# Optimization experiments

Measured on AMD Instinct MI355X. Metric: run time of the kernel, lower is better.

The kernel has to match this reference:

```python
import jax, jax.numpy as jnp
import numpy as np

B, H, W = 512, 15, 15
DF, DP, DV, DD = 64, 32, 64, 32
PM = 16
NUM_LINE = 442503  # get_total_num_line_encoding(11)


def fake_quant(x, scale=128., num_bits=8, floor=False):
    qmin = float(-(2 ** (num_bits - 1)))
    qmax = float(2 ** (num_bits - 1) - 1)
    xs = jnp.clip(x * scale, qmin, qmax)
    q = jnp.floor(xs) if floor else jnp.round(xs)
    q = xs + jax.lax.stop_gradient(q - xs)  # straight-through estimator
    return q / scale


def qw(w):  # LinearBlock quant=True weight: int8 at scale 128
    return fake_quant(w, 128., 8)


def qb(b):  # LinearBlock quant=True bias: int32 at scale 128*128
    return fake_quant(b, 128. * 128., 32)


def setup_inputs() -> dict:
    key = jax.random.key(0)
    ks = jax.random.split(key, 24)
    n = lambda k, shape, s=0.1: jax.random.normal(k, shape, dtype=jnp.float32) * s
    return {
        'line_encoding': jax.random.randint(ks[0], (B, 4, H, W), 0, NUM_LINE, dtype=jnp.int32),
        'emb': n(ks[1], (NUM_LINE, DF), 0.5),
        'dw_w': n(ks[2], (DD, 3, 3)),
        'dw_b': n(ks[3], (DD,)),
        'pw1_w': n(ks[4], (DP * 2, DF)), 'pw1_b': n(ks[5], (DP * 2,)),
        'pw2_w': n(ks[6], (PM * DP + PM, DP * 2)), 'pw2_b': n(ks[7], (PM * DP + PM,)),
        'pout_w': n(ks[8], (PM,), 0.2), 'pout_b': n(ks[9], (1,), 0.2),
        'star_up1_w': n(ks[10], (4, DV, DF)), 'star_up1_b': n(ks[11], (4, DV)),
        'star_up2_w': n(ks[12], (4, DV, DF)), 'star_up2_b': n(ks[13], (4, DV)),
        'star_down_w': n(ks[14], (4, DV, DV)), 'star_down_b': n(ks[15], (4, DV)),
        'vl1_w': n(ks[16], (DV, DF + 4 * DV)), 'vl1_b': n(ks[17], (DV,)),
        'vl2_w': n(ks[18], (DV, DV)), 'vl2_b': n(ks[19], (DV,)),
        'vl3_w': n(ks[20], (3, DV)), 'vl3_b': n(ks[21], (3,)),
    }


def _star(x, w1, b1, w2, b2, w3, b3):
    # x: [B,R,DF]; weights [R,DV,DF] (per-region parameter gather)
    x1 = jnp.einsum('brc,rdc->brd', x, qw(w1)) + qb(b1)[None]
    x2 = jnp.einsum('brc,rdc->brd', x, qw(w2)) + qb(b2)[None]
    h = jax.nn.relu(x1) * x2  # star operation
    return jnp.einsum('brc,rdc->brd', h, qw(w3)) + qb(b3)[None]


def _forward(line_encoding, emb, dw_w, dw_b, pw1_w, pw1_b, pw2_w, pw2_b,
             pout_w, pout_b, star_up1_w, star_up1_b, star_up2_w, star_up2_b,
             star_down_w, star_down_b, vl1_w, vl1_b, vl2_w, vl2_b, vl3_w, vl3_b):
    # ---- feature: embedding gather + quant + direction mean ----
    f = emb[line_encoding]                       # [B,4,H,W,DF]
    f = jnp.clip(f, -16., 16.)
    f = fake_quant(f, 32., 16)
    f = jax.nn.relu(jnp.mean(f, axis=1))         # [B,H,W,DF]
    f = jnp.transpose(f, (0, 3, 1, 2))           # [B,DF,H,W]
    # ---- depthwise 3x3 conv, quant='pixel-dwconv-floor' ----
    x = fake_quant(f[:, :DD] * 4., 128., 16)
    wq = fake_quant(dw_w, 65536., 16)
    bq = fake_quant(dw_b, 128., 16)
    xp = jnp.pad(x, ((0, 0), (0, 0), (1, 1), (1, 1)))
    pat = jnp.stack([xp[:, :, dy:dy + H, dx:dx + W]
                     for dy in range(3) for dx in range(3)], axis=2)  # [B,DD,9,H,W]
    prod = fake_quant(pat * wq.reshape(1, DD, 9, 1, 1), 128., 32, floor=True)
    conv = jax.nn.relu(prod.sum(axis=2) + bq.reshape(1, DD, 1, 1))
    feat_dw = fake_quant(conv, 128., 16)
    feat_dir = fake_quant(f[:, DD:], 128., 16)
    feature = jnp.concatenate([feat_dw, feat_dir], axis=1)  # [B,DF,H,W]
    # ---- global and 3x3 regional sums ----
    feature_sum = fake_quant(feature.sum(axis=(2, 3)) / 256., 128., 32, floor=True)
    Hs = [0, H // 3 + (H % 3 == 2), H // 3 * 2 + (H % 3 > 0), H]
    Ws = [0, W // 3 + (W % 3 == 2), W // 3 * 2 + (W % 3 > 0), W]
    regions = jnp.stack([feature[:, :, Hs[i]:Hs[i + 1], Ws[j]:Ws[j + 1]].sum(axis=(2, 3))
                         for i in range(3) for j in range(3)], axis=1)  # [B,9,DF]
    regions = fake_quant(regions / 32., 128., 32, floor=True)
    # ---- policy: dynamic per-sample pointwise conv ----
    h = jax.nn.relu(feature_sum @ qw(pw1_w).T + qb(pw1_b))
    o = h @ qw(pw2_w).T + qb(pw2_b)                         # [B, PM*DP+PM]
    pw = fake_quant(o[:, :PM * DP], 128. * 128., 16, floor=True).reshape(-1, PM, DP)
    pin = fake_quant(feature[:, :DP], 128., 16)             # [B,DP,H,W]
    pol = jnp.einsum('bchw,bic->bihw', pin, pw)             # grouped conv, groups=B
    pbias = o[:, PM * DP:].reshape(-1, PM, 1, 1)
    pol = jax.nn.relu(pol + pbias)
    policy = jnp.einsum('bihw,i->bhw', pol, pout_w)[:, None] + pout_b[0]  # [B,1,H,W]
    # ---- value: corner/edge/center star blocks over 9 regions ----
    idx = jnp.array([0, 1, 0, 1, 2, 1, 0, 1, 0])  # 0=corner,1=edge,2=center
    v = _star(regions, star_up1_w[idx], star_up1_b[idx], star_up2_w[idx],
              star_up2_b[idx], star_down_w[idx], star_down_b[idx])  # [B,9,DV]
    fq8 = lambda t: fake_quant(t, 128., 8, floor=True)
    def avg4(a, b, c, d):
        a, b, c, d = fq8(a), fq8(b), fq8(c), fq8(d)
        ab = fq8((a + b + 1. / 128.) / 2.)
        cd = fq8((c + d + 1. / 128.) / 2.)
        return fq8((ab + cd + 1. / 128.) / 2.)
    quads = jnp.stack([avg4(v[:, 0], v[:, 1], v[:, 3], v[:, 4]),
                       avg4(v[:, 1], v[:, 2], v[:, 4], v[:, 5]),
                       avg4(v[:, 3], v[:, 4], v[:, 6], v[:, 7]),
                       avg4(v[:, 4], v[:, 5], v[:, 7], v[:, 8])], axis=1)  # [B,4,DV]
    qidx = jnp.array([3, 3, 3, 3])  # value_quad shared across quadrants
    vq = _star(quads, star_up1_w[qidx], star_up1_b[qidx], star_up2_w[qidx],
               star_up2_b[qidx], star_down_w[qidx], star_down_b[qidx])  # [B,4,DV]
    value = jnp.concatenate([feature_sum, vq.reshape(vq.shape[0], -1)], axis=1)  # [B,320]
    value = jax.nn.relu(value @ qw(vl1_w).T + qb(vl1_b))
    value = jax.nn.relu(value @ qw(vl2_w).T + qb(vl2_b))
    value = value @ qw(vl3_w).T + qb(vl3_b)                 # [B,3]
    return value, policy


def reference(line_encoding, emb, dw_w, dw_b, pw1_w, pw1_b, pw2_w, pw2_b,
              pout_w, pout_b, star_up1_w, star_up1_b, star_up2_w, star_up2_b,
              star_down_w, star_down_b, vl1_w, vl1_b, vl2_w, vl2_b, vl3_w, vl3_b):
    return _forward(line_encoding, emb, dw_w, dw_b, pw1_w, pw1_b, pw2_w, pw2_b,
                    pout_w, pout_b, star_up1_w, star_up1_b, star_up2_w, star_up2_b,
                    star_down_w, star_down_b, vl1_w, vl1_b, vl2_w, vl2_b, vl3_w, vl3_b)
```

## Files before the change

kernel.cpp:

```cpp
#include <hip/hip_runtime.h>

#define NPOS 225
#define FSTR 227

__device__ __forceinline__ float qw8(float w) {
  return rintf(fminf(fmaxf(w * 128.f, -128.f), 127.f)) * 0.0078125f;
}
__device__ __forceinline__ float qb32(float b) {
  return rintf(b * 16384.f) * 6.103515625e-05f;
}
__device__ __forceinline__ float fq8f(float v) {
  return floorf(fminf(fmaxf(v * 128.f, -128.f), 127.f)) * 0.0078125f;
}
__device__ __forceinline__ float qdir(float v) {
  return rintf(fminf(fmaxf(v, -16.f), 16.f) * 32.f) * 0.03125f;
}

__global__ __launch_bounds__(256, 2)
void nnue_fused(const int* __restrict__ line,
                const float* __restrict__ emb,
                const float* __restrict__ dw_w,  const float* __restrict__ dw_b,
                const float* __restrict__ pw1_w, const float* __restrict__ pw1_b,
                const float* __restrict__ pw2_w, const float* __restrict__ pw2_b,
                const float* __restrict__ pout_w,const float* __restrict__ pout_b,
                const float* __restrict__ su1w,  const float* __restrict__ su1b,
                const float* __restrict__ su2w,  const float* __restrict__ su2b,
                const float* __restrict__ sdw,   const float* __restrict__ sdb,
                const float* __restrict__ vl1w,  const float* __restrict__ vl1b,
                const float* __restrict__ vl2w,  const float* __restrict__ vl2b,
                const float* __restrict__ vl3w,  const float* __restrict__ vl3b,
                float* __restrict__ out)
{
  __shared__ float fbuf[64 * FSTR];
  __shared__ float sreg[9 * 64];
  __shared__ float sfsum[64];
  __shared__ float shh[64];
  __shared__ float sobuf[528];
  __shared__ float spwq[512];
  __shared__ float hstar[9 * 64];
  __shared__ float vstar[9 * 64];
  __shared__ float squads[4 * 64];
  __shared__ float shq[4 * 64];
  __shared__ float svq[4 * 64];
  __shared__ float sv1[64];
  __shared__ float sv2[64];

  const int tid  = threadIdx.x;
  const int b    = blockIdx.x;
  const int wid  = tid >> 6;
  const int lane = tid & 63;
  const int* le  = line + b * 4 * NPOS;

  for (int p = wid; p < NPOS; p += 8) {
    const int p2 = p + 4;
    const bool h2 = (p2 < NPOS);
    int i0 = le[p], i1 = le[NPOS + p], i2 = le[2 * NPOS + p], i3 = le[3 * NPOS + p];
    int j0 = i0, j1 = i1, j2 = i2, j3 = i3;
    if (h2) { j0 = le[p2]; j1 = le[NPOS + p2]; j2 = le[2 * NPOS + p2]; j3 = le[3 * NPOS + p2]; }
    float a0 = emb[i0 * 64 + lane], a1 = emb[i1 * 64 + lane];
    float a2 = emb[i2 * 64 + lane], a3 = emb[i3 * 64 + lane];
    float c0 = emb[j0 * 64 + lane], c1 = emb[j1 * 64 + lane];
    float c2 = emb[j2 * 64 + lane], c3 = emb[j3 * 64 + lane];
    fbuf[lane * FSTR + p] = fmaxf((qdir(a0) + qdir(a1) + qdir(a2) + qdir(a3)) * 0.25f, 0.f);
    if (h2)
      fbuf[lane * FSTR + p2] = fmaxf((qdir(c0) + qdir(c1) + qdir(c2) + qdir(c3)) * 0.25f, 0.f);
  }
  __syncthreads();

  {
    const int cc = tid >> 3;
    const int pg = tid & 7;
    float wq9[9];
#pragma unroll
    for (int t = 0; t < 9; ++t)
      wq9[t] = rintf(fminf(fmaxf(dw_w[cc * 9 + t] * 65536.f, -32768.f), 32767.f)) * 1.52587890625e-05f;
    const float bq = rintf(fminf(fmaxf(dw_b[cc] * 128.f, -32768.f), 32767.f)) * 0.0078125f;
    float outr[29];
#pragma unroll
    for (int k = 0; k < 29; ++k) {
      const int p = pg + 8 * k;
      if (p < NPOS) {
        const int y0 = p / 15, x0 = p - y0 * 15;
        float s = 0.f;
#pragma unroll
        for (int dy = 0; dy < 3; ++dy)
#pragma unroll
          for (int dx = 0; dx < 3; ++dx) {
            const int y = y0 + dy - 1, x = x0 + dx - 1;
            float xv = 0.f;
            if ((unsigned)y < 15u && (unsigned)x < 15u) xv = 4.f * fbuf[cc * FSTR + y * 15 + x];
            s += floorf(xv * wq9[dy * 3 + dx] * 128.f) * 0.0078125f;
          }
        s = fmaxf(s + bq, 0.f);
        outr[k] = fminf(s, 255.9921875f);
      } else outr[k] = 0.f;
    }
    __syncthreads();
#pragma unroll
    for (int k = 0; k < 29; ++k) {
      const int p = pg + 8 * k;
      if (p < NPOS) fbuf[cc * FSTR + p] = outr[k];
    }
  }
  __syncthreads();

  if (tid < 64) {
    float tot = 0.f;
#pragma unroll
    for (int rh = 0; rh < 3; ++rh)
#pragma unroll
      for (int rw = 0; rw < 3; ++rw) {
        float rs = 0.f;
        for (int y = rh * 5; y < rh * 5 + 5; ++y)
          for (int x = rw * 5; x < rw * 5 + 5; ++x)
            rs += fbuf[tid * FSTR + y * 15 + x];
        sreg[(rh * 3 + rw) * 64 + tid] = floorf(rs * 4.f) * 0.0078125f;
        tot += rs;
      }
    sfsum[tid] = floorf(tot * 0.5f) * 0.0078125f;
  }
  __syncthreads();

  if (tid < 64) {
    const float4* wr = (const float4*)(pw1_w + tid * 64);
    float acc = 0.f;
#pragma unroll
    for (int c4 = 0; c4 < 16; ++c4) {
      float4 w = wr[c4];
      acc += sfsum[c4 * 4 + 0] * qw8(w.x);
      acc += sfsum[c4 * 4 + 1] * qw8(w.y);
      acc += sfsum[c4 * 4 + 2] * qw8(w.z);
      acc += sfsum[c4 * 4 + 3] * qw8(w.w);
    }
    acc += qb32(pw1_b[tid]);
    shh[tid] = fmaxf(acc, 0.f);
  }
  __syncthreads();
  for (int j = tid; j < 528; j += 256) {
    const float4* wr = (const float4*)(pw2_w + j * 64);
    float acc = 0.f;
#pragma unroll
    for (int c4 = 0; c4 < 16; ++c4) {
      float4 w = wr[c4];
      acc += shh[c4 * 4 + 0] * qw8(w.x);
      acc += shh[c4 * 4 + 1] * qw8(w.y);
      acc += shh[c4 * 4 + 2] * qw8(w.z);
      acc += shh[c4 * 4 + 3] * qw8(w.w);
    }
    acc += qb32(pw2_b[j]);
    sobuf[j] = acc;
    if (j < 512)
      spwq[j] = floorf(fminf(fmaxf(acc * 16384.f, -32768.f), 32767.f)) * 6.103515625e-05f;
  }
  __syncthreads();

  if (tid < NPOS) {
    float pinv[32];
#pragma unroll
    for (int c = 0; c < 32; ++c) pinv[c] = fbuf[c * FSTR + tid];
    float acc = 0.f;
#pragma unroll
    for (int i = 0; i < 16; ++i) {
      float s = 0.f;
#pragma unroll
      for (int c = 0; c < 32; ++c) s += pinv[c] * spwq[i * 32 + c];
      s = fmaxf(s + sobuf[512 + i], 0.f);
      acc += s * pout_w[i];
    }
    out[1536 + b * NPOS + tid] = acc + pout_b[0];
  }

  {
    const int g = tid >> 6;
    const int d = tid & 63;
    int ty, rA, rB, rC, rD;
    if (g == 0)      { ty = 0; rA = 0; rB = 2; rC = 6; rD = 8; }
    else if (g == 1) { ty = 1; rA = 1; rB = 3; rC = 5; rD = 7; }
    else             { ty = 2; rA = 4; rB = 4; rC = 4; rD = 4; }
    const float4* w1r = (const float4*)(su1w + ty * 4096 + d * 64);
    const float4* w2r = (const float4*)(su2w + ty * 4096 + d * 64);
    float aA1 = 0, aB1 = 0, aC1 = 0, aD1 = 0, aA2 = 0, aB2 = 0, aC2 = 0, aD2 = 0;
#pragma unroll 4
    for (int c4 = 0; c4 < 16; ++c4) {
      float4 w1 = w1r[c4], w2 = w2r[c4];
      float q1[4] = {qw8(w1.x), qw8(w1.y), qw8(w1.z), qw8(w1.w)};
      float q2[4] = {qw8(w2.x), qw8(w2.y), qw8(w2.z), qw8(w2.w)};
#pragma unroll
      for (int u = 0; u < 4; ++u) {
        const int c = c4 * 4 + u;
        float xA = sreg[rA * 64 + c], xB = sreg[rB * 64 + c];
        float xC = sreg[rC * 64 + c], xD = sreg[rD * 64 + c];
        aA1 += xA * q1[u]; aB1 += xB * q1[u]; aC1 += xC * q1[u]; aD1 += xD * q1[u];
        aA2 += xA * q2[u]; aB2 += xB * q2[u]; aC2 += xC * q2[u]; aD2 += xD * q2[u];
      }
    }
    const float bb1 = qb32(su1b[ty * 64 + d]);
    const float bb2 = qb32(su2b[ty * 64 + d]);
    hstar[rA * 64 + d] = fmaxf(aA1 + bb1, 0.f) * (aA2 + bb2);
    hstar[rB * 64 + d] = fmaxf(aB1 + bb1, 0.f) * (aB2 + bb2);
    hstar[rC * 64 + d] = fmaxf(aC1 + bb1, 0.f) * (aC2 + bb2);
    hstar[rD * 64 + d] = fmaxf(aD1 + bb1, 0.f) * (aD2 + bb2);
    __syncthreads();
    const float4* wdr = (const float4*)(sdw + ty * 4096 + d * 64);
    float dA = 0, dB = 0, dC = 0, dD = 0;
#pragma unroll 4
    for (int c4 = 0; c4 < 16; ++c4) {
      float4 w = wdr[c4];
      float q[4] = {qw8(w.x), qw8(w.y), qw8(w.z), qw8(w.w)};
#pragma unroll
      for (int u = 0; u < 4; ++u) {
        const int c = c4 * 4 + u;
        dA += hstar[rA * 64 + c] * q[u]; dB += hstar[rB * 64 + c] * q[u];
        dC += hstar[rC * 64 + c] * q[u]; dD += hstar[rD * 64 + c] * q[u];
      }
    }
    const float bd = qb32(sdb[ty * 64 + d]);
    vstar[rA * 64 + d] = dA + bd;
    vstar[rB * 64 + d] = dB + bd;
    vstar[rC * 64 + d] = dC + bd;
    vstar[rD * 64 + d] = dD + bd;
  }
  __syncthreads();

  {
    const int g = tid >> 6, d = tid & 63;
    int r0, r1, r2v, r3v;
    if (g == 0)      { r0 = 0; r1 = 1; r2v = 3; r3v = 4; }
    else if (g == 1) { r0 = 1; r1 = 2; r2v = 4; r3v = 5; }
    else if (g == 2) { r0 = 3; r1 = 4; r2v = 6; r3v = 7; }
    else             { r0 = 4; r1 = 5; r2v = 7; r3v = 8; }
    float a  = fq8f(vstar[r0 * 64 + d]);
    float bb = fq8f(vstar[r1 * 64 + d]);
    float cc = fq8f(vstar[r2v * 64 + d]);
    float dd = fq8f(vstar[r3v * 64 + d]);
    float ab = fq8f((a + bb + 0.0078125f) * 0.5f);
    float cd = fq8f((cc + dd + 0.0078125f) * 0.5f);
    squads[g * 64 + d] = fq8f((ab + cd + 0.0078125f) * 0.5f);
  }
  __syncthreads();

  {
    const int g = tid >> 6, d = tid & 63;
    const float4* w1r = (const float4*)(su1w + 3 * 4096 + d * 64);
    const float4* w2r = (const float4*)(su2w + 3 * 4096 + d * 64);
    float a1 = 0.f, a2 = 0.f;
#pragma unroll 4
    for (int c4 = 0; c4 < 16; ++c4) {
      float4 w1 = w1r[c4], w2 = w2r[c4];
      float q1[4] = {qw8(w1.x), qw8(w1.y), qw8(w1.z), qw8(w1.w)};
      float q2[4] = {qw8(w2.x), qw8(w2.y), qw8(w2.z), qw8(w2.w)};
#pragma unroll
      for (int u = 0; u < 4; ++u) {
        float xq = squads[g * 64 + c4 * 4 + u];
        a1 += xq * q1[u];
        a2 += xq * q2[u];
      }
    }
    shq[g * 64 + d] = fmaxf(a1 + qb32(su1b[192 + d]), 0.f) * (a2 + qb32(su2b[192 + d]));
    __syncthreads();
    const float4* wdr = (const float4*)(sdw + 3 * 4096 + d * 64);
    float ad = 0.f;
#pragma unroll 4
    for (int c4 = 0; c4 < 16; ++c4) {
      float4 w = wdr[c4];
      float q[4] = {qw8(w.x), qw8(w.y), qw8(w.z), qw8(w.w)};
#pragma unroll
      for (int u = 0; u < 4; ++u) ad += shq[g * 64 + c4 * 4 + u] * q[u];
    }
    svq[g * 64 + d] = ad + qb32(sdb[192 + d]);
  }
  __syncthreads();

  if (tid < 64) {
    const float4* wr = (const float4*)(vl1w + tid * 320);
    float acc = 0.f;
#pragma unroll 4
    for (int k4 = 0; k4 < 16; ++k4) {
      float4 w = wr[k4];
      acc += sfsum[k4 * 4 + 0] * qw8(w.x);
      acc += sfsum[k4 * 4 + 1] * qw8(w.y);
      acc += sfsum[k4 * 4 + 2] * qw8(w.z);
      acc += sfsum[k4 * 4 + 3] * qw8(w.w);
    }
#pragma unroll 4
    for (int k4 = 16; k4 < 80; ++k4) {
      float4 w = wr[k4];
      const int base = k4 * 4 - 64;
      acc += svq[base + 0] * qw8(w.x);
      acc += svq[base + 1] * qw8(w.y);
      acc += svq[base + 2] * qw8(w.z);
      acc += svq[base + 3] * qw8(w.w);
    }
    acc += qb32(vl1b[tid]);
    sv1[tid] = fmaxf(acc, 0.f);
  }
  __syncthreads();
  if (tid < 64) {
    const float4* wr = (const float4*)(vl2w + tid * 64);
    float acc = 0.f;
#pragma unroll 4
    for (int k4 = 0; k4 < 16; ++k4) {
      float4 w = wr[k4];
      acc += sv1[k4 * 4 + 0] * qw8(w.x);
      acc += sv1[k4 * 4 + 1] * qw8(w.y);
      acc += sv1[k4 * 4 + 2] * qw8(w.z);
      acc += sv1[k4 * 4 + 3] * qw8(w.w);
    }
    acc += qb32(vl2b[tid]);
    sv2[tid] = fmaxf(acc, 0.f);
  }
  __syncthreads();
  if (tid < 3) {
    const float* wr = vl3w + tid * 64;
    float acc = 0.f;
#pragma unroll
    for (int k = 0; k < 64; ++k) acc += sv2[k] * qw8(wr[k]);
    out[b * 3 + tid] = acc + qb32(vl3b[tid]);
  }
}

extern "C" void kernel_launch(void* const* d_in, const int* in_sizes, int n_in,
                              void* d_out, int out_size, void* d_ws, size_t ws_size,
                              hipStream_t stream) {
  (void)in_sizes; (void)n_in; (void)out_size; (void)d_ws; (void)ws_size;
  nnue_fused<<<512, 256, 0, stream>>>(
      (const int*)d_in[0],  (const float*)d_in[1],
      (const float*)d_in[2],  (const float*)d_in[3],
      (const float*)d_in[4],  (const float*)d_in[5],
      (const float*)d_in[6],  (const float*)d_in[7],
      (const float*)d_in[8],  (const float*)d_in[9],
      (const float*)d_in[10], (const float*)d_in[11],
      (const float*)d_in[12], (const float*)d_in[13],
      (const float*)d_in[14], (const float*)d_in[15],
      (const float*)d_in[16], (const float*)d_in[17],
      (const float*)d_in[18], (const float*)d_in[19],
      (const float*)d_in[20], (const float*)d_in[21],
      (float*)d_out);
}
```

Before: 285.2 us.

## Pre-quantize weights in a prep kernel and switch feature map to integer ushort

Adds a prep kernel that quantizes all weights and biases into a workspace once per call, so the main kernel no longer repeats the quantization math in every block. The feature map moves from float to unsigned short fixed-point, and the depthwise conv becomes integer arithmetic. This halves shared memory use and allows 3 blocks per CU. The embedding gather is batched using indices staged in LDS with readfirstlane, and the region sums are spread across all threads. The cost is an extra kernel launch, and the exactness of the integer rewrite depends on the fixed-point equivalences holding.

```diff
diff --git a/kernel.cpp b/kernel.cpp
--- a/kernel.cpp
+++ b/kernel.cpp
@@ -1,7 +1,27 @@
 #include <hip/hip_runtime.h>
 
 #define NPOS 225
-#define FSTR 227
+#define FSTR 226
+
+#define OFF_PW1Q 0
+#define OFF_PW2Q 4096
+#define OFF_SU1Q 37888
+#define OFF_SU2Q 54272
+#define OFF_SDQ  70656
+#define OFF_VL1Q 87040
+#define OFF_VL2Q 107520
+#define OFF_VL3Q 111616
+#define OFF_PW1B 111808
+#define OFF_PW2B 111872
+#define OFF_SU1B 112400
+#define OFF_SU2B 112656
+#define OFF_SDB  112912
+#define OFF_VL1B 113168
+#define OFF_VL2B 113232
+#define OFF_VL3B 113296
+#define OFF_DWW  113300
+#define OFF_DWB  113588
+#define WS_TOTAL 113620
 
 __device__ __forceinline__ float qw8(float w) {
   return rintf(fminf(fmaxf(w * 128.f, -128.f), 127.f)) * 0.0078125f;
@@ -12,36 +32,70 @@
 __device__ __forceinline__ float fq8f(float v) {
   return floorf(fminf(fmaxf(v * 128.f, -128.f), 127.f)) * 0.0078125f;
 }
-__device__ __forceinline__ float qdir(float v) {
-  return rintf(fminf(fmaxf(v, -16.f), 16.f) * 32.f) * 0.03125f;
-}
-
-__global__ __launch_bounds__(256, 2)
-void nnue_fused(const int* __restrict__ line,
-                const float* __restrict__ emb,
-                const float* __restrict__ dw_w,  const float* __restrict__ dw_b,
-                const float* __restrict__ pw1_w, const float* __restrict__ pw1_b,
-                const float* __restrict__ pw2_w, const float* __restrict__ pw2_b,
-                const float* __restrict__ pout_w,const float* __restrict__ pout_b,
-                const float* __restrict__ su1w,  const float* __restrict__ su1b,
-                const float* __restrict__ su2w,  const float* __restrict__ su2b,
-                const float* __restrict__ sdw,   const float* __restrict__ sdb,
-                const float* __restrict__ vl1w,  const float* __restrict__ vl1b,
-                const float* __restrict__ vl2w,  const float* __restrict__ vl2b,
-                const float* __restrict__ vl3w,  const float* __restrict__ vl3b,
-                float* __restrict__ out)
+__device__ __forceinline__ float qd32(float v) {
+  return rintf(fminf(fmaxf(v, -16.f), 16.f) * 32.f);
+}
+
+__global__ void nnue_prep(const float* __restrict__ pw1_w, const float* __restrict__ pw1_b,
+                          const float* __restrict__ pw2_w, const float* __restrict__ pw2_b,
+                          const float* __restrict__ su1w,  const float* __restrict__ su1b,
+                          const float* __restrict__ su2w,  const float* __restrict__ su2b,
+                          const float* __restrict__ sdw,   const float* __restrict__ sdb,
+                          const float* __restrict__ vl1w,  const float* __restrict__ vl1b,
+                          const float* __restrict__ vl2w,  const float* __restrict__ vl2b,
+                          const float* __restrict__ vl3w,  const float* __restrict__ vl3b,
+                          const float* __restrict__ dw_w,  const float* __restrict__ dw_b,
+                          float* __restrict__ wsf, int* __restrict__ wsi)
 {
-  __shared__ float fbuf[64 * FSTR];
-  __shared__ float sreg[9 * 64];
+  const int i = blockIdx.x * 256 + threadIdx.x;
+  if (i < 111808) {
+    const float* src; int off;
+    if      (i < 4096)   { src = pw1_w; off = 0; }
+    else if (i < 37888)  { src = pw2_w; off = 4096; }
+    else if (i < 54272)  { src = su1w;  off = 37888; }
+    else if (i < 70656)  { src = su2w;  off = 54272; }
+    else if (i < 87040)  { src = sdw;   off = 70656; }
+    else if (i < 107520) { src = vl1w;  off = 87040; }
+    else if (i < 111616) { src = vl2w;  off = 107520; }
+    else                 { src = vl3w;  off = 111616; }
+    wsf[i] = qw8(src[i - off]);
+  } else if (i < 113299) {
+    const int j = i - 111808;
+    const float* src; int off;
+    if      (j < 64)   { src = pw1_b; off = 0; }
+    else if (j < 592)  { src = pw2_b; off = 64; }
+    else if (j < 848)  { src = su1b;  off = 592; }
+    else if (j < 1104) { src = su2b;  off = 848; }
+    else if (j < 1360) { src = sdb;   off = 1104; }
+    else if (j < 1424) { src = vl1b;  off = 1360; }
+    else if (j < 1488) { src = vl2b;  off = 1424; }
+    else               { src = vl3b;  off = 1488; }
+    wsf[i] = qb32(src[j - off]);
+  } else if (i >= 113300 && i < 113588) {
+    wsi[i] = (int)rintf(fminf(fmaxf(dw_w[i - 113300] * 65536.f, -32768.f), 32767.f));
+  } else if (i >= 113588 && i < 113620) {
+    wsi[i] = (int)rintf(fminf(fmaxf(dw_b[i - 113588] * 128.f, -32768.f), 32767.f));
+  }
+}
+
+__global__ __launch_bounds__(256, 3)
+void nnue_main(const int* __restrict__ line, const float* __restrict__ emb,
+               const float* __restrict__ pout_w, const float* __restrict__ pout_b,
+               const float* __restrict__ wsf, const int* __restrict__ wsi,
+               float* __restrict__ out)
+{
+  __shared__ unsigned short fbuf[64 * FSTR];
+  __shared__ int sle[900];
+  __shared__ float sreg[576];
   __shared__ float sfsum[64];
   __shared__ float shh[64];
   __shared__ float sobuf[528];
   __shared__ float spwq[512];
-  __shared__ float hstar[9 * 64];
-  __shared__ float vstar[9 * 64];
-  __shared__ float squads[4 * 64];
-  __shared__ float shq[4 * 64];
-  __shared__ float svq[4 * 64];
+  __shared__ float hstar[576];
+  __shared__ float vstar[576];
+  __shared__ float squads[256];
+  __shared__ float shq[256];
+  __shared__ float svq[256];
   __shared__ float sv1[64];
   __shared__ float sv2[64];
 
@@ -51,103 +105,132 @@
   const int lane = tid & 63;
   const int* le  = line + b * 4 * NPOS;
 
-  for (int p = wid; p < NPOS; p += 8) {
-    const int p2 = p + 4;
-    const bool h2 = (p2 < NPOS);
-    int i0 = le[p], i1 = le[NPOS + p], i2 = le[2 * NPOS + p], i3 = le[3 * NPOS + p];
-    int j0 = i0, j1 = i1, j2 = i2, j3 = i3;
-    if (h2) { j0 = le[p2]; j1 = le[NPOS + p2]; j2 = le[2 * NPOS + p2]; j3 = le[3 * NPOS + p2]; }
-    float a0 = emb[i0 * 64 + lane], a1 = emb[i1 * 64 + lane];
-    float a2 = emb[i2 * 64 + lane], a3 = emb[i3 * 64 + lane];
-    float c0 = emb[j0 * 64 + lane], c1 = emb[j1 * 64 + lane];
-    float c2 = emb[j2 * 64 + lane], c3 = emb[j3 * 64 + lane];
-    fbuf[lane * FSTR + p] = fmaxf((qdir(a0) + qdir(a1) + qdir(a2) + qdir(a3)) * 0.25f, 0.f);
-    if (h2)
-      fbuf[lane * FSTR + p2] = fmaxf((qdir(c0) + qdir(c1) + qdir(c2) + qdir(c3)) * 0.25f, 0.f);
+  for (int i = tid; i < 900; i += 256) sle[i] = le[i];
+  __syncthreads();
+
+  const int start = (wid * NPOS) >> 2;
+  const int end   = ((wid + 1) * NPOS) >> 2;
+  for (int p0 = start; p0 < end; p0 += 8) {
+    float vv[32];
+#pragma unroll
+    for (int j = 0; j < 8; ++j) {
+      int pp = p0 + j; if (pp >= end) pp = end - 1;
+#pragma unroll
+      for (int d = 0; d < 4; ++d) {
+        const int idx = __builtin_amdgcn_readfirstlane(sle[d * NPOS + pp]);
+        vv[j * 4 + d] = emb[(size_t)(unsigned)idx * 64u + (unsigned)lane];
+      }
+    }
+#pragma unroll
+    for (int j = 0; j < 8; ++j) {
+      const int pp = p0 + j;
+      if (pp < end) {
+        float s = qd32(vv[4 * j]) + qd32(vv[4 * j + 1]) + qd32(vv[4 * j + 2]) + qd32(vv[4 * j + 3]);
+        fbuf[lane * FSTR + pp] = (unsigned short)fmaxf(s, 0.f);
+      }
+    }
   }
   __syncthreads();
 
   {
     const int cc = tid >> 3;
     const int pg = tid & 7;
-    float wq9[9];
-#pragma unroll
-    for (int t = 0; t < 9; ++t)
-      wq9[t] = rintf(fminf(fmaxf(dw_w[cc * 9 + t] * 65536.f, -32768.f), 32767.f)) * 1.52587890625e-05f;
-    const float bq = rintf(fminf(fmaxf(dw_b[cc] * 128.f, -32768.f), 32767.f)) * 0.0078125f;
-    float outr[29];
+    int w9[9];
+#pragma unroll
+    for (int t = 0; t < 9; ++t) w9[t] = wsi[OFF_DWW + cc * 9 + t];
+    const int bqi = wsi[OFF_DWB + cc];
+    const unsigned short* frow = &fbuf[cc * FSTR];
+    int outr[29];
 #pragma unroll
     for (int k = 0; k < 29; ++k) {
       const int p = pg + 8 * k;
+      int res = 0;
       if (p < NPOS) {
-        const int y0 = p / 15, x0 = p - y0 * 15;
-        float s = 0.f;
-#pragma unroll
-        for (int dy = 0; dy < 3; ++dy)
+        const int y0 = (p * 2185) >> 15;
+        const int x0 = p - y0 * 15;
+        const int ym = (y0 > 0), yp = (y0 < 14), xm = (x0 > 0), xp = (x0 < 14);
+        int acc = 0;
+#pragma unroll
+        for (int dy = 0; dy < 3; ++dy) {
+          const int vy = (dy == 0) ? ym : ((dy == 2) ? yp : 1);
 #pragma unroll
           for (int dx = 0; dx < 3; ++dx) {
-            const int y = y0 + dy - 1, x = x0 + dx - 1;
-            float xv = 0.f;
-            if ((unsigned)y < 15u && (unsigned)x < 15u) xv = 4.f * fbuf[cc * FSTR + y * 15 + x];
-            s += floorf(xv * wq9[dy * 3 + dx] * 128.f) * 0.0078125f;
+            const int vx = (dx == 0) ? xm : ((dx == 2) ? xp : 1);
+            int q = p + (dy - 1) * 15 + (dx - 1);
+            q = (q < 0) ? 0 : ((q > 224) ? 224 : q);
+            int kk = frow[q];
+            kk = (vy && vx) ? kk : 0;
+            acc += (kk * 4 * w9[dy * 3 + dx]) >> 16;
           }
-        s = fmaxf(s + bq, 0.f);
-        outr[k] = fminf(s, 255.9921875f);
-      } else outr[k] = 0.f;
+        }
+        res = acc + bqi;
+        res = res < 0 ? 0 : res;
+        res = res > 32767 ? 32767 : res;
+      }
+      outr[k] = res;
     }
     __syncthreads();
 #pragma unroll
     for (int k = 0; k < 29; ++k) {
       const int p = pg + 8 * k;
-      if (p < NPOS) fbuf[cc * FSTR + p] = outr[k];
-    }
-  }
-  __syncthreads();
-
+      if (p < NPOS) fbuf[cc * FSTR + p] = (unsigned short)outr[k];
+    }
+  }
+  __syncthreads();
+
+  {
+    int* sregKi = (int*)sreg;
+    for (int task = tid; task < 576; task += 256) {
+      const int r = task >> 6, c = task & 63;
+      const int rh = (r * 11) >> 5;
+      const int rw = r - rh * 3;
+      const unsigned short* fr = &fbuf[c * FSTR + rh * 75 + rw * 5];
+      int K = 0;
+#pragma unroll
+      for (int y = 0; y < 5; ++y)
+#pragma unroll
+        for (int x = 0; x < 5; ++x) K += fr[y * 15 + x];
+      sregKi[task] = K;
+    }
+  }
+  __syncthreads();
   if (tid < 64) {
-    float tot = 0.f;
-#pragma unroll
-    for (int rh = 0; rh < 3; ++rh)
-#pragma unroll
-      for (int rw = 0; rw < 3; ++rw) {
-        float rs = 0.f;
-        for (int y = rh * 5; y < rh * 5 + 5; ++y)
-          for (int x = rw * 5; x < rw * 5 + 5; ++x)
-            rs += fbuf[tid * FSTR + y * 15 + x];
-        sreg[(rh * 3 + rw) * 64 + tid] = floorf(rs * 4.f) * 0.0078125f;
-        tot += rs;
-      }
-    sfsum[tid] = floorf(tot * 0.5f) * 0.0078125f;
+    int* sregKi = (int*)sreg;
+    int Ks[9], tot = 0;
+#pragma unroll
+    for (int r = 0; r < 9; ++r) { Ks[r] = sregKi[r * 64 + tid]; tot += Ks[r]; }
+#pragma unroll
+    for (int r = 0; r < 9; ++r) sreg[r * 64 + tid] = (float)(Ks[r] >> 5) * 0.0078125f;
+    sfsum[tid] = (float)(tot >> 8) * 0.0078125f;
   }
   __syncthreads();
 
   if (tid < 64) {
-    const float4* wr = (const float4*)(pw1_w + tid * 64);
+    const float4* wr = (const float4*)(wsf + OFF_PW1Q + tid * 64);
     float acc = 0.f;
 #pragma unroll
     for (int c4 = 0; c4 < 16; ++c4) {
       float4 w = wr[c4];
-      acc += sfsum[c4 * 4 + 0] * qw8(w.x);
-      acc += sfsum[c4 * 4 + 1] * qw8(w.y);
-      acc += sfsum[c4 * 4 + 2] * qw8(w.z);
-      acc += sfsum[c4 * 4 + 3] * qw8(w.w);
-    }
-    acc += qb32(pw1_b[tid]);
-    shh[tid] = fmaxf(acc, 0.f);
+      acc += sfsum[c4 * 4 + 0] * w.x;
+      acc += sfsum[c4 * 4 + 1] * w.y;
+      acc += sfsum[c4 * 4 + 2] * w.z;
+      acc += sfsum[c4 * 4 + 3] * w.w;
+    }
+    shh[tid] = fmaxf(acc + wsf[OFF_PW1B + tid], 0.f);
   }
   __syncthreads();
   for (int j = tid; j < 528; j += 256) {
-    const float4* wr = (const float4*)(pw2_w + j * 64);
+    const float4* wr = (const float4*)(wsf + OFF_PW2Q + j * 64);
     float acc = 0.f;
 #pragma unroll
     for (int c4 = 0; c4 < 16; ++c4) {
       float4 w = wr[c4];
-      acc += shh[c4 * 4 + 0] * qw8(w.x);
-      acc += shh[c4 * 4 + 1] * qw8(w.y);
-      acc += shh[c4 * 4 + 2] * qw8(w.z);
-      acc += shh[c4 * 4 + 3] * qw8(w.w);
-    }
-    acc += qb32(pw2_b[j]);
+      acc += shh[c4 * 4 + 0] * w.x;
+      acc += shh[c4 * 4 + 1] * w.y;
+      acc += shh[c4 * 4 + 2] * w.z;
+      acc += shh[c4 * 4 + 3] * w.w;
+    }
+    acc += wsf[OFF_PW2B + j];
     sobuf[j] = acc;
     if (j < 512)
       spwq[j] = floorf(fminf(fmaxf(acc * 16384.f, -32768.f), 32767.f)) * 6.103515625e-05f;
@@ -157,7 +240,7 @@
   if (tid < NPOS) {
     float pinv[32];
 #pragma unroll
-    for (int c = 0; c < 32; ++c) pinv[c] = fbuf[c * FSTR + tid];
+    for (int c = 0; c < 32; ++c) pinv[c] = (float)fbuf[c * FSTR + tid] * 0.0078125f;
     float acc = 0.f;
 #pragma unroll
     for (int i = 0; i < 16; ++i) {
@@ -177,14 +260,14 @@
     if (g == 0)      { ty = 0; rA = 0; rB = 2; rC = 6; rD = 8; }
     else if (g == 1) { ty = 1; rA = 1; rB = 3; rC = 5; rD = 7; }
     else             { ty = 2; rA = 4; rB = 4; rC = 4; rD = 4; }
-    const float4* w1r = (const float4*)(su1w + ty * 4096 + d * 64);
-    const float4* w2r = (const float4*)(su2w + ty * 4096 + d * 64);
+    const float4* w1r = (const float4*)(wsf + OFF_SU1Q + ty * 4096 + d * 64);
+    const float4* w2r = (const float4*)(wsf + OFF_SU2Q + ty * 4096 + d * 64);
     float aA1 = 0, aB1 = 0, aC1 = 0, aD1 = 0, aA2 = 0, aB2 = 0, aC2 = 0, aD2 = 0;
 #pragma unroll 4
     for (int c4 = 0; c4 < 16; ++c4) {
       float4 w1 = w1r[c4], w2 = w2r[c4];
-      float q1[4] = {qw8(w1.x), qw8(w1.y), qw8(w1.z), qw8(w1.w)};
-      float q2[4] = {qw8(w2.x), qw8(w2.y), qw8(w2.z), qw8(w2.w)};
+      float q1[4] = {w1.x, w1.y, w1.z, w1.w};
+      float q2[4] = {w2.x, w2.y, w2.z, w2.w};
 #pragma unroll
       for (int u = 0; u < 4; ++u) {
         const int c = c4 * 4 + u;
@@ -194,19 +277,19 @@
         aA2 += xA * q2[u]; aB2 += xB * q2[u]; aC2 += xC * q2[u]; aD2 += xD * q2[u];
       }
     }
-    const float bb1 = qb32(su1b[ty * 64 + d]);
-    const float bb2 = qb32(su2b[ty * 64 + d]);
+    const float bb1 = wsf[OFF_SU1B + ty * 64 + d];
+    const float bb2 = wsf[OFF_SU2B + ty * 64 + d];
     hstar[rA * 64 + d] = fmaxf(aA1 + bb1, 0.f) * (aA2 + bb2);
     hstar[rB * 64 + d] = fmaxf(aB1 + bb1, 0.f) * (aB2 + bb2);
     hstar[rC * 64 + d] = fmaxf(aC1 + bb1, 0.f) * (aC2 + bb2);
     hstar[rD * 64 + d] = fmaxf(aD1 + bb1, 0.f) * (aD2 + bb2);
     __syncthreads();
-    const float4* wdr = (const float4*)(sdw + ty * 4096 + d * 64);
+    const float4* wdr = (const float4*)(wsf + OFF_SDQ + ty * 4096 + d * 64);
     float dA = 0, dB = 0, dC = 0, dD = 0;
 #pragma unroll 4
     for (int c4 = 0; c4 < 16; ++c4) {
       float4 w = wdr[c4];
-      float q[4] = {qw8(w.x), qw8(w.y), qw8(w.z), qw8(w.w)};
+      float q[4] = {w.x, w.y, w.z, w.w};
 #pragma unroll
       for (int u = 0; u < 4; ++u) {
         const int c = c4 * 4 + u;
@@ -214,7 +297,7 @@
         dC += hstar[rC * 64 + c] * q[u]; dD += hstar[rD * 64 + c] * q[u];
       }
     }
-    const float bd = qb32(sdb[ty * 64 + d]);
+    const float bd = wsf[OFF_SDB + ty * 64 + d];
     vstar[rA * 64 + d] = dA + bd;
     vstar[rB * 64 + d] = dB + bd;
     vstar[rC * 64 + d] = dC + bd;
@@ -241,99 +324,96 @@
 
   {
     const int g = tid >> 6, d = tid & 63;
-    const float4* w1r = (const float4*)(su1w + 3 * 4096 + d * 64);
-    const float4* w2r = (const float4*)(su2w + 3 * 4096 + d * 64);
+    const float4* w1r = (const float4*)(wsf + OFF_SU1Q + 3 * 4096 + d * 64);
+    const float4* w2r = (const float4*)(wsf + OFF_SU2Q + 3 * 4096 + d * 64);
     float a1 = 0.f, a2 = 0.f;
 #pragma unroll 4
     for (int c4 = 0; c4 < 16; ++c4) {
       float4 w1 = w1r[c4], w2 = w2r[c4];
-      float q1[4] = {qw8(w1.x), qw8(w1.y), qw8(w1.z), qw8(w1.w)};
-      float q2[4] = {qw8(w2.x), qw8(w2.y), qw8(w2.z), qw8(w2.w)};
-#pragma unroll
-      for (int u = 0; u < 4; ++u) {
-        float xq = squads[g * 64 + c4 * 4 + u];
-        a1 += xq * q1[u];
-        a2 += xq * q2[u];
-      }
-    }
-    shq[g * 64 + d] = fmaxf(a1 + qb32(su1b[192 + d]), 0.f) * (a2 + qb32(su2b[192 + d]));
+      float xq0 = squads[g * 64 + c4 * 4 + 0], xq1 = squads[g * 64 + c4 * 4 + 1];
+      float xq2 = squads[g * 64 + c4 * 4 + 2], xq3 = squads[g * 64 + c4 * 4 + 3];
+      a1 += xq0 * w1.x + xq1 * w1.y + xq2 * w1.z + xq3 * w1.w;
+      a2 += xq0 * w2.x + xq1 * w2.y + xq2 * w2.z + xq3 * w2.w;
+    }
+    shq[g * 64 + d] = fmaxf(a1 + wsf[OFF_SU1B + 192 + d], 0.f) * (a2 + wsf[OFF_SU2B + 192 + d]);
     __syncthreads();
-    const float4* wdr = (const float4*)(sdw + 3 * 4096 + d * 64);
+    const float4* wdr = (const float4*)(wsf + OFF_SDQ + 3 * 4096 + d * 64);
     float ad = 0.f;
 #pragma unroll 4
     for (int c4 = 0; c4 < 16; ++c4) {
       float4 w = wdr[c4];
-      float q[4] = {qw8(w.x), qw8(w.y), qw8(w.z), qw8(w.w)};
-#pragma unroll
-      for (int u = 0; u < 4; ++u) ad += shq[g * 64 + c4 * 4 + u] * q[u];
-    }
-    svq[g * 64 + d] = ad + qb32(sdb[192 + d]);
+      ad += shq[g * 64 + c4 * 4 + 0] * w.x + shq[g * 64 + c4 * 4 + 1] * w.y
+          + shq[g * 64 + c4 * 4 + 2] * w.z + shq[g * 64 + c4 * 4 + 3] * w.w;
+    }
+    svq[g * 64 + d] = ad + wsf[OFF_SDB + 192 + d];
   }
   __syncthreads();
 
   if (tid < 64) {
-    const float4* wr = (const float4*)(vl1w + tid * 320);
+    const float4* wr = (const float4*)(wsf + OFF_VL1Q + tid * 320);
     float acc = 0.f;
 #pragma unroll 4
     for (int k4 = 0; k4 < 16; ++k4) {
       float4 w = wr[k4];
-      acc += sfsum[k4 * 4 + 0] * qw8(w.x);
-      acc += sfsum[k4 * 4 + 1] * qw8(w.y);
-      acc += sfsum[k4 * 4 + 2] * qw8(w.z);
-      acc += sfsum[k4 * 4 + 3] * qw8(w.w);
+      acc += sfsum[k4 * 4 + 0] * w.x;
+      acc += sfsum[k4 * 4 + 1] * w.y;
+      acc += sfsum[k4 * 4 + 2] * w.z;
+      acc += sfsum[k4 * 4 + 3] * w.w;
     }
 #pragma unroll 4
     for (int k4 = 16; k4 < 80; ++k4) {
       float4 w = wr[k4];
       const int base = k4 * 4 - 64;
-      acc += svq[base + 0] * qw8(w.x);
-      acc += svq[base + 1] * qw8(w.y);
-      acc += svq[base + 2] * qw8(w.z);
-      acc += svq[base + 3] * qw8(w.w);
-    }
-    acc += qb32(vl1b[tid]);
-    sv1[tid] = fmaxf(acc, 0.f);
+      acc += svq[base + 0] * w.x;
+      acc += svq[base + 1] * w.y;
+      acc += svq[base + 2] * w.z;
+      acc += svq[base + 3] * w.w;
+    }
+    sv1[tid] = fmaxf(acc + wsf[OFF_VL1B + tid], 0.f);
   }
   __syncthreads();
   if (tid < 64) {
-    const float4* wr = (const float4*)(vl2w + tid * 64);
+    const float4* wr = (const float4*)(wsf + OFF_VL2Q + tid * 64);
     float acc = 0.f;
 #pragma unroll 4
     for (int k4 = 0; k4 < 16; ++k4) {
       float4 w = wr[k4];
-      acc += sv1[k4 * 4 + 0] * qw8(w.x);
-      acc += sv1[k4 * 4 + 1] * qw8(w.y);
-      acc += sv1[k4 * 4 + 2] * qw8(w.z);
-      acc += sv1[k4 * 4 + 3] * qw8(w.w);
-    }
-    acc += qb32(vl2b[tid]);
-    sv2[tid] = fmaxf(acc, 0.f);
+      acc += sv1[k4 * 4 + 0] * w.x;
+      acc += sv1[k4 * 4 + 1] * w.y;
+      acc += sv1[k4 * 4 + 2] * w.z;
+      acc += sv1[k4 * 4 + 3] * w.w;
+    }
+    sv2[tid] = fmaxf(acc + wsf[OFF_VL2B + tid], 0.f);
   }
   __syncthreads();
   if (tid < 3) {
-    const float* wr = vl3w + tid * 64;
-    float acc = 0.f;
-#pragma unroll
-    for (int k = 0; k < 64; ++k) acc += sv2[k] * qw8(wr[k]);
-    out[b * 3 + tid] = acc + qb32(vl3b[tid]);
+    const float* wr = wsf + OFF_VL3Q + tid * 64;
+    float acc = 0.f;
+#pragma unroll
+    for (int k = 0; k < 64; ++k) acc += sv2[k] * wr[k];
+    out[b * 3 + tid] = acc + wsf[OFF_VL3B + tid];
   }
 }
 
 extern "C" void kernel_launch(void* const* d_in, const int* in_sizes, int n_in,
                               void* d_out, int out_size, void* d_ws, size_t ws_size,
                               hipStream_t stream) {
-  (void)in_sizes; (void)n_in; (void)out_size; (void)d_ws; (void)ws_size;
-  nnue_fused<<<512, 256, 0, stream>>>(
-      (const int*)d_in[0],  (const float*)d_in[1],
-      (const float*)d_in[2],  (const float*)d_in[3],
+  (void)in_sizes; (void)n_in; (void)out_size; (void)ws_size;
+  float* wsf = (float*)d_ws;
+  int*   wsi = (int*)d_ws;
+  nnue_prep<<<(WS_TOTAL + 255) / 256, 256, 0, stream>>>(
       (const float*)d_in[4],  (const float*)d_in[5],
       (const float*)d_in[6],  (const float*)d_in[7],
-      (const float*)d_in[8],  (const float*)d_in[9],
       (const float*)d_in[10], (const float*)d_in[11],
       (const float*)d_in[12], (const float*)d_in[13],
       (const float*)d_in[14], (const float*)d_in[15],
       (const float*)d_in[16], (const float*)d_in[17],
       (const float*)d_in[18], (const float*)d_in[19],
       (const float*)d_in[20], (const float*)d_in[21],
-      (float*)d_out);
-}
+      (const float*)d_in[2],  (const float*)d_in[3],
+      wsf, wsi);
+  nnue_main<<<512, 256, 0, stream>>>(
+      (const int*)d_in[0], (const float*)d_in[1],
+      (const float*)d_in[8], (const float*)d_in[9],
+      wsf, wsi, (float*)d_out);
+}
```

Measured after the change: 260.1 us. 1.1x faster.
